# Performance work log

Hardware: AMD Instinct MI355X
Metric: run time of the kernel (lower is better)

Reference implementation:

```python
import jax, jax.numpy as jnp
import numpy as np

NEG_SLOPE = 0.01  # LeakyReLU default
STRIDE = 5        # group_length // 4
EPS = 1e-5        # RMSNorm eps


def leaky_relu(x):
    return jnp.where(x >= 0, x, NEG_SLOPE * x)


def rmsnorm(x, w):
    return x * jax.lax.rsqrt(jnp.mean(x * x, axis=-1, keepdims=True) + EPS) * w


def s6(x, fc1_w, fc1_b, fc2_w, fc2_b, fc3_w, fc3_b, A):
    # x: [B, L, D] with D = 2*d_model; A: [D, N]
    delta = jax.nn.softplus(x @ fc1_w.T + fc1_b)        # [B, L, D]
    Bm = x @ fc2_w.T + fc2_b                             # [B, L, N]
    Cm = x @ fc3_w.T + fc3_b                             # [B, L, N]
    dA = jnp.exp(jnp.einsum('bld,dn->bldn', delta, A))   # [B, L, D, N]
    dBx = jnp.einsum('bld,bln,bld->bldn', delta, Bm, x)  # delta * B * x

    def step(h, inp):
        dA_t, dBx_t = inp
        h = dA_t * h + dBx_t
        return h, h

    B_, L, D, N = dA.shape
    h0 = jnp.zeros((B_, D, N), dtype=x.dtype)
    _, hs = jax.lax.scan(step, h0, (jnp.swapaxes(dA, 0, 1), jnp.swapaxes(dBx, 0, 1)))
    hs = jnp.swapaxes(hs, 0, 1)                          # [B, L, D, N]
    return jnp.einsum('bln,bldn->bld', Cm, hs)           # [B, L, D]


def setup_inputs() -> dict:
    key = jax.random.key(0)
    ks = iter(jax.random.split(key, 32))

    def rn(shape, scale=0.02):
        return scale * jax.random.normal(next(ks), shape, dtype=jnp.float32)

    B, band, gl, d, N, L = 256, 189, 20, 128, 128, 34
    di = 2 * d
    return {
        'x': jax.random.normal(next(ks), (B, 1, band), dtype=jnp.float32),
        'conv_w': rn((d, 1, gl)), 'conv_b': rn((d,)),
        'norm_w': jnp.ones((d,), jnp.float32),
        'inp_w': rn((di, d)), 'inp_b': rn((di,)),
        'seqconv_w': rn((L, L, 3)), 'seqconv_b': rn((L,)),
        'convlin_w': rn((di, di)), 'convlin_b': rn((di,)),
        'fc1_w': rn((di, di)), 'fc1_b': rn((di,)),
        'fc2_w': rn((N, di)), 'fc2_b': rn((N,)),
        'fc3_w': rn((N, di)), 'fc3_b': rn((N,)),
        'A': jnp.ones((di, N), jnp.float32) / jnp.sqrt(jnp.float32(N)),
        'D_w': rn((di, d)), 'D_b': rn((di,)),
        'out_w': rn((d, di)), 'out_b': rn((d,)),
        'fnn1_w': rn((64, L * d)), 'fnn1_b': rn((64,)),
        'fnn2_w': rn((32, 64)), 'fnn2_b': rn((32,)),
    }


def reference(x, conv_w, conv_b, norm_w, inp_w, inp_b, seqconv_w, seqconv_b,
              convlin_w, convlin_b, fc1_w, fc1_b, fc2_w, fc2_b, fc3_w, fc3_b,
              A, D_w, D_b, out_w, out_b, fnn1_w, fnn1_b, fnn2_w, fnn2_b):
    # group division: Conv1d(1, d, k=20, stride=5) + LeakyReLU
    g = jax.lax.conv_general_dilated(x, conv_w, (STRIDE,), [(0, 0)],
                                     dimension_numbers=('NCH', 'OIH', 'NCH'))
    g = leaky_relu(g + conv_b[None, :, None])            # [B, d, L]
    h = jnp.swapaxes(g, 1, 2)                            # [B, L, d]
    # Mamba block
    xn = rmsnorm(h, norm_w)
    xp = xn @ inp_w.T + inp_b                            # [B, L, 2d]
    # Conv1d(seq_len, seq_len, k=3, pad=1): seq axis L is the channel dim
    xc = jax.lax.conv_general_dilated(xp, seqconv_w, (1,), [(1, 1)],
                                      dimension_numbers=('NCH', 'OIH', 'NCH'))
    xc = jax.nn.silu(xc + seqconv_b[None, :, None])
    xc = xc @ convlin_w.T + convlin_b                    # [B, L, 2d]
    xs = s6(xc, fc1_w, fc1_b, fc2_w, fc2_b, fc3_w, fc3_b, A)
    y = jax.nn.silu(xs) * jax.nn.silu(xn @ D_w.T + D_b)  # gated
    y = y @ out_w.T + out_b                              # [B, L, d]
    # FNN head
    f = y.reshape(y.shape[0], -1)                        # [B, L*d]
    f = leaky_relu(f @ fnn1_w.T + fnn1_b)
    return f @ fnn2_w.T + fnn2_b                         # [B, 32]
```

## Files before the change

kernel.cpp:

```cpp
#include <hip/hip_runtime.h>
#include <math.h>


#define NB    256
#define LL    34
#define DD    128
#define DI    256
#define NN    128
#define MM    (NB*LL)

using u16 = unsigned short;
typedef __attribute__((ext_vector_type(8))) short short8;
typedef __attribute__((ext_vector_type(4))) float f32x4;

__device__ __forceinline__ float silu_f(float x)  { return x / (1.f + __expf(-x)); }
__device__ __forceinline__ float softplus_f(float x) {
    return fmaxf(x, 0.f) + __logf(1.f + __expf(-fabsf(x)));
}
__device__ __forceinline__ float leaky_f(float x) { return (x >= 0.f) ? x : 0.01f * x; }

__device__ __forceinline__ u16 f2bf(float x) {
    unsigned u = __float_as_uint(x);
    return (u16)((u + 0x7FFF + ((u >> 16) & 1)) >> 16);
}
__device__ __forceinline__ float bf2f(u16 h) {
    return __uint_as_float(((unsigned)h) << 16);
}
__device__ __forceinline__ void f2pair(float v, u16* h, u16* l) {
    u16 hh = f2bf(v);
    *h = hh;
    *l = f2bf(v - bf2f(hh));
}

__global__ __launch_bounds__(256)
void prep_k(const float* __restrict__ inp_w, const float* __restrict__ D_w,
            const float* __restrict__ fc1_w, const float* __restrict__ fc2_w,
            const float* __restrict__ fc3_w, const float* __restrict__ convlin_w,
            const float* __restrict__ out_w,
            const float* __restrict__ inp_b, const float* __restrict__ D_b,
            const float* __restrict__ fc1_b, const float* __restrict__ fc2_b,
            const float* __restrict__ fc3_b,
            const float* __restrict__ W1, const float* __restrict__ A,
            u16* __restrict__ wc1h, u16* __restrict__ wc1l,
            u16* __restrict__ wc3h, u16* __restrict__ wc3l,
            u16* __restrict__ cvh,  u16* __restrict__ cvl,
            u16* __restrict__ owh,  u16* __restrict__ owl,
            float* __restrict__ bias1, float* __restrict__ bias3,
            float* __restrict__ W1T, int* __restrict__ flag)
{
    const int bx  = blockIdx.x;
    const int tid = threadIdx.x;
    __shared__ float tile[64][65];

    if (bx < 1152) {
        int i = bx * 256 + tid;
        if (i < 65536) {
            float v = (i < 32768) ? inp_w[i] : D_w[i - 32768];
            f2pair(v, &wc1h[i], &wc1l[i]);
        } else if (i < 196608) {
            int j = i - 65536;
            float v = (j < 65536) ? fc1_w[j] : (j < 98304 ? fc2_w[j - 65536] : fc3_w[j - 98304]);
            f2pair(v, &wc3h[j], &wc3l[j]);
        } else if (i < 262144) {
            int j = i - 196608;
            f2pair(convlin_w[j], &cvh[j], &cvl[j]);
        } else if (i < 294912) {
            int j = i - 262144;
            f2pair(out_w[j], &owh[j], &owl[j]);
        }
        if (i < 512)  bias1[i] = (i < 256) ? inp_b[i] : D_b[i - 256];
        else if (i < 1024) {
            int j = i - 512;
            bias3[j] = (j < 256) ? fc1_b[j] : (j < 384 ? fc2_b[j - 256] : fc3_b[j - 384]);
        }
    } else if (bx < 1220) {
        const int bt = bx - 1152;
        for (int p = 0; p < 16; p++) {
            int idx = tid + p * 256;
            int r = idx >> 6, c = idx & 63;
            tile[r][c] = W1[(size_t)r * 4352 + bt * 64 + c];
        }
        __syncthreads();
        for (int p = 0; p < 16; p++) {
            int idx = tid + p * 256;
            int cc = idx >> 6, rr = idx & 63;
            W1T[(size_t)(bt * 64 + cc) * 64 + rr] = tile[rr][cc];
        }
    } else {
        __shared__ int s;
        if (tid == 0) s = 1;
        __syncthreads();
        bool ok = true;
        for (int k = 0; k < 128; k++) {
            int idx = tid + k * 256;
            ok &= (A[idx] == A[idx & ~127]);
        }
        if (!ok) s = 0;
        __syncthreads();
        if (tid == 0) *flag = s;
    }
}

__global__ __launch_bounds__(1024, 1)
void mega2_k(const int* __restrict__ flag,
             const float* __restrict__ x,
             const float* __restrict__ cw, const float* __restrict__ cb,
             const float* __restrict__ nw,
             const u16* __restrict__ wc1h, const u16* __restrict__ wc1l,
             const float* __restrict__ bias1,
             const float* __restrict__ scw, const float* __restrict__ scb,
             const u16* __restrict__ cvh, const u16* __restrict__ cvl,
             const float* __restrict__ clb,
             const u16* __restrict__ wc3h, const u16* __restrict__ wc3l,
             const float* __restrict__ bias3,
             const float* __restrict__ A,
             const u16* __restrict__ owh, const u16* __restrict__ owl,
             const float* __restrict__ outb,
             float* __restrict__ buf1,
             float* __restrict__ buf3,
             u16* __restrict__ bcpair,
             u16* __restrict__ xc2h, u16* __restrict__ xc2l,
             float* __restrict__ fout)
{
    const int b    = blockIdx.x;
    const int tid  = threadIdx.x;
    const int wave = tid >> 6;
    const int lane = tid & 63;
    const int l15  = lane & 15;
    const int lq   = lane >> 4;

    __shared__ __align__(16) char smem[144944];
    float (*sx)[264] = (float (*)[264])(smem);
    float (*sw)[112] = (float (*)[112])(smem + 35904);
    u16 (*sXch)[264] = (u16 (*)[264])(smem);
    u16 (*sXcl)[264] = (u16 (*)[264])(smem + 25344);
    u16 (*sBh)[136]  = (u16 (*)[136])(smem);
    u16 (*sBl)[136]  = (u16 (*)[136])(smem + 13056);
    u16 (*sCh)[136]  = (u16 (*)[136])(smem + 26112);
    u16 (*sCl)[136]  = (u16 (*)[136])(smem + 39168);
    u16 (*sGh)[264]  = (u16 (*)[264])(smem);
    u16 (*sGl)[264]  = (u16 (*)[264])(smem + 25344);
    u16 (*sXnh)[136] = (u16 (*)[136])(smem + 52224);
    u16 (*sXnl)[136] = (u16 (*)[136])(smem + 65280);
    u16 (*sX2h)[264] = (u16 (*)[264])(smem + 52224);
    u16 (*sX2l)[264] = (u16 (*)[264])(smem + 77568);
    float (*sM)[49]  = (float (*)[49])(smem + 102912);
    float (*sDG)[260]= (float (*)[260])(smem + 109584);

    const bool uni = (*flag != 0);

    for (int idx = tid; idx < LL * LL * 3; idx += 1024) {
        int lo = idx / 102;
        int rem = idx - lo * 102;
        int li = rem / 3;
        int k  = rem - li * 3;
        sw[li][lo * 3 + k] = scw[idx];
    }
    if (tid < LL) { sx[tid][0] = 0.f; sx[tid][257] = 0.f; }

    {
        const int t = lane;
        #pragma unroll
        for (int pass = 0; pass < 3; pass++) {
            const int rr = pass * 16 + wave;
            if (rr < LL) {
                const float* xr = x + (size_t)b * 189 + rr * 5;
                float xv[20];
                #pragma unroll
                for (int k = 0; k < 20; k++) xv[k] = xr[k];
                float g0 = cb[t];
                float g1 = cb[t + 64];
                #pragma unroll
                for (int k = 0; k < 20; k++) {
                    g0 = fmaf(xv[k], cw[t * 20 + k], g0);
                    g1 = fmaf(xv[k], cw[(t + 64) * 20 + k], g1);
                }
                g0 = leaky_f(g0);
                g1 = leaky_f(g1);
                float s = fmaf(g1, g1, g0 * g0);
                #pragma unroll
                for (int m = 32; m >= 1; m >>= 1) s += __shfl_xor(s, m);
                float inv = 1.f / sqrtf(s * (1.f / 128.f) + 1e-5f);
                float v0 = g0 * inv * nw[t];
                float v1 = g1 * inv * nw[t + 64];
                f2pair(v0, &sXnh[rr][t], &sXnl[rr][t]);
                f2pair(v1, &sXnh[rr][t + 64], &sXnl[rr][t + 64]);
            }
        }
    }
    __syncthreads();

    {
        const int c0 = wave * 32;
        f32x4 a1[3][2];
        #pragma unroll
        for (int i = 0; i < 3; i++)
            #pragma unroll
            for (int j = 0; j < 2; j++) a1[i][j] = (f32x4){0.f, 0.f, 0.f, 0.f};

        #pragma unroll
        for (int ks = 0; ks < 4; ks++) {
            short8 fh[3], fl[3];
            #pragma unroll
            for (int i = 0; i < 3; i++) {
                fh[i] = *(const short8*)&sXnh[i * 16 + l15][ks * 32 + lq * 8];
                fl[i] = *(const short8*)&sXnl[i * 16 + l15][ks * 32 + lq * 8];
            }
            #pragma unroll
            for (int j = 0; j < 2; j++) {
                const size_t wo = (size_t)(c0 + j * 16 + l15) * 128 + ks * 32 + lq * 8;
                short8 bh = *(const short8*)&wc1h[wo];
                short8 bl = *(const short8*)&wc1l[wo];
                #pragma unroll
                for (int i = 0; i < 3; i++) {
                    a1[i][j] = __builtin_amdgcn_mfma_f32_16x16x32_bf16(fh[i], bh, a1[i][j], 0, 0, 0);
                    a1[i][j] = __builtin_amdgcn_mfma_f32_16x16x32_bf16(fh[i], bl, a1[i][j], 0, 0, 0);
                    a1[i][j] = __builtin_amdgcn_mfma_f32_16x16x32_bf16(fl[i], bh, a1[i][j], 0, 0, 0);
                }
            }
        }
        #pragma unroll
        for (int i = 0; i < 3; i++) {
            int row = i * 16 + lq * 4;
            #pragma unroll
            for (int j = 0; j < 2; j++) {
                int col = c0 + j * 16 + l15;
                float bb = bias1[col];
                #pragma unroll
                for (int r = 0; r < 4; r++) {
                    float v = a1[i][j][r] + bb;
                    int rr = row + r;
                    if (rr < LL) {
                        if (col < 256) {
                            sx[rr][col + 1] = v;
                        } else {
                            sDG[rr][col - 256] = v;
                            if (!uni)
                                buf1[((size_t)b * LL + rr) * 512 + col] = v;
                        }
                    }
                }
            }
        }
    }
    __syncthreads();

    {
        const int tx  = tid & 63;
        const int ty  = tid >> 6;
        const int j0c = tx * 4;
        const int cbase = (ty < 2) ? ty * 3 : 6 + (ty - 2) * 2;
        const int ccnt  = (ty < 2) ? 3 : 2;

        float cacc[3][4];
        #pragma unroll
        for (int i = 0; i < 3; i++)
            #pragma unroll
            for (int jj = 0; jj < 4; jj++) cacc[i][jj] = 0.f;

        for (int li = 0; li < LL; li++) {
            float4 xa = *(const float4*)&sx[li][j0c];
            float2 xb = *(const float2*)&sx[li][j0c + 4];
            float xv[6] = {xa.x, xa.y, xa.z, xa.w, xb.x, xb.y};
            const float* swr = &sw[li][0];
            #pragma unroll
            for (int i = 0; i < 3; i++) {
                if (i < ccnt) {
                    int lo3 = (cbase + i) * 3;
                    float w0 = swr[lo3 + 0];
                    float w1 = swr[lo3 + 1];
                    float w2 = swr[lo3 + 2];
                    #pragma unroll
                    for (int jj = 0; jj < 4; jj++) {
                        cacc[i][jj] = fmaf(w0, xv[jj],     cacc[i][jj]);
                        cacc[i][jj] = fmaf(w1, xv[jj + 1], cacc[i][jj]);
                        cacc[i][jj] = fmaf(w2, xv[jj + 2], cacc[i][jj]);
                    }
                }
            }
        }
        __syncthreads();

        #pragma unroll
        for (int i = 0; i < 3; i++) {
            if (i < ccnt) {
                int lo = cbase + i;
                float bb = scb[lo];
                ushort4 oh, ol;
                float v0 = silu_f(cacc[i][0] + bb);
                float v1 = silu_f(cacc[i][1] + bb);
                float v2 = silu_f(cacc[i][2] + bb);
                float v3 = silu_f(cacc[i][3] + bb);
                f2pair(v0, &oh.x, &ol.x);
                f2pair(v1, &oh.y, &ol.y);
                f2pair(v2, &oh.z, &ol.z);
                f2pair(v3, &oh.w, &ol.w);
                *(ushort4*)&sXch[lo][j0c] = oh;
                *(ushort4*)&sXcl[lo][j0c] = ol;
            }
        }
    }
    __syncthreads();

    {
        const int c0 = wave * 16;
        f32x4 a2[3];
        #pragma unroll
        for (int i = 0; i < 3; i++) a2[i] = (f32x4){0.f, 0.f, 0.f, 0.f};

        #pragma unroll
        for (int ks = 0; ks < 8; ks++) {
            short8 fh[3], fl[3];
            #pragma unroll
            for (int i = 0; i < 3; i++) {
                fh[i] = *(const short8*)&sXch[i * 16 + l15][ks * 32 + lq * 8];
                fl[i] = *(const short8*)&sXcl[i * 16 + l15][ks * 32 + lq * 8];
            }
            const size_t wo = (size_t)(c0 + l15) * 256 + ks * 32 + lq * 8;
            short8 bh = *(const short8*)&cvh[wo];
            short8 bl = *(const short8*)&cvl[wo];
            #pragma unroll
            for (int i = 0; i < 3; i++) {
                a2[i] = __builtin_amdgcn_mfma_f32_16x16x32_bf16(fh[i], bh, a2[i], 0, 0, 0);
                a2[i] = __builtin_amdgcn_mfma_f32_16x16x32_bf16(fh[i], bl, a2[i], 0, 0, 0);
                a2[i] = __builtin_amdgcn_mfma_f32_16x16x32_bf16(fl[i], bh, a2[i], 0, 0, 0);
            }
        }
        #pragma unroll
        for (int i = 0; i < 3; i++) {
            int row = i * 16 + lq * 4;
            int col = c0 + l15;
            float bb = clb[col];
            #pragma unroll
            for (int r = 0; r < 4; r++) {
                float v = a2[i][r] + bb;
                u16 hh, ll;
                f2pair(v, &hh, &ll);
                sX2h[row + r][col] = hh;
                sX2l[row + r][col] = ll;
                if (!uni && (row + r) < LL) {
                    xc2h[(size_t)(b * LL + row + r) * 256 + col] = hh;
                    xc2l[(size_t)(b * LL + row + r) * 256 + col] = ll;
                }
            }
        }
    }
    __syncthreads();

    {
        const int c0 = wave * 32;
        f32x4 a3[3][2];
        #pragma unroll
        for (int i = 0; i < 3; i++)
            #pragma unroll
            for (int j = 0; j < 2; j++) a3[i][j] = (f32x4){0.f, 0.f, 0.f, 0.f};

        #pragma unroll
        for (int ks = 0; ks < 8; ks++) {
            short8 fh[3], fl[3];
            #pragma unroll
            for (int i = 0; i < 3; i++) {
                fh[i] = *(const short8*)&sX2h[i * 16 + l15][ks * 32 + lq * 8];
                fl[i] = *(const short8*)&sX2l[i * 16 + l15][ks * 32 + lq * 8];
            }
            #pragma unroll
            for (int j = 0; j < 2; j++) {
                const size_t wo = (size_t)(c0 + j * 16 + l15) * 256 + ks * 32 + lq * 8;
                short8 bh = *(const short8*)&wc3h[wo];
                short8 bl = *(const short8*)&wc3l[wo];
                #pragma unroll
                for (int i = 0; i < 3; i++) {
                    a3[i][j] = __builtin_amdgcn_mfma_f32_16x16x32_bf16(fh[i], bh, a3[i][j], 0, 0, 0);
                    a3[i][j] = __builtin_amdgcn_mfma_f32_16x16x32_bf16(fh[i], bl, a3[i][j], 0, 0, 0);
                    a3[i][j] = __builtin_amdgcn_mfma_f32_16x16x32_bf16(fl[i], bh, a3[i][j], 0, 0, 0);
                }
            }
        }
        #pragma unroll
        for (int i = 0; i < 3; i++) {
            int row = i * 16 + lq * 4;
            #pragma unroll
            for (int j = 0; j < 2; j++) {
                int col = c0 + j * 16 + l15;
                float bb = bias3[col];
                #pragma unroll
                for (int r = 0; r < 4; r++) {
                    float v = a3[i][j][r] + bb;
                    int rr = row + r;
                    if (col < 256) {
                        v = softplus_f(v);
                        if (rr < LL) buf3[((size_t)b * LL + rr) * 512 + col] = v;
                    } else {
                        u16 hh, ll;
                        f2pair(v, &hh, &ll);
                        int cc = col & 127;
                        if (col < 384) { sBh[rr][cc] = hh; sBl[rr][cc] = ll; }
                        else           { sCh[rr][cc] = hh; sCl[rr][cc] = ll; }
                        if (!uni && rr < LL) {
                            buf3[((size_t)b * LL + rr) * 512 + col] = v;
                            u16* rb = bcpair + ((size_t)b * LL + rr) * 1024
                                      + ((col < 384) ? 0 : 256) + cc;
                            rb[0]   = hh;
                            rb[128] = ll;
                        }
                    }
                }
            }
        }
    }
    __syncthreads();
    if (!uni) return;

    float u[LL], eS[LL];
    if (tid < 256) {
        const int d = tid;
        const float a_d = A[(size_t)d * NN];
        const float* pDel = buf3 + (size_t)b * LL * 512 + d;
        float S = 0.f;
        #pragma unroll
        for (int l = 0; l < LL; l++) {
            float dl = pDel[l * 512];
            S = fmaf(dl, a_d, S);
            eS[l] = __expf(S);
            float xv = bf2f(sX2h[l][d]) + bf2f(sX2l[l][d]);
            u[l] = __expf(-S) * dl * xv;
        }
    } else if (wave >= 4 && wave < 13) {
        int tt = wave - 4;
        int ti = tt / 3, tj = tt - ti * 3;
        f32x4 acc = (f32x4){0.f, 0.f, 0.f, 0.f};
        #pragma unroll
        for (int ks = 0; ks < 4; ks++) {
            short8 ch = *(const short8*)&sCh[ti * 16 + l15][ks * 32 + lq * 8];
            short8 cl = *(const short8*)&sCl[ti * 16 + l15][ks * 32 + lq * 8];
            short8 bh = *(const short8*)&sBh[tj * 16 + l15][ks * 32 + lq * 8];
            short8 bl = *(const short8*)&sBl[tj * 16 + l15][ks * 32 + lq * 8];
            acc = __builtin_amdgcn_mfma_f32_16x16x32_bf16(ch, bh, acc, 0, 0, 0);
            acc = __builtin_amdgcn_mfma_f32_16x16x32_bf16(ch, bl, acc, 0, 0, 0);
            acc = __builtin_amdgcn_mfma_f32_16x16x32_bf16(cl, bh, acc, 0, 0, 0);
        }
        #pragma unroll
        for (int r = 0; r < 4; r++) {
            int row = ti * 16 + lq * 4 + r;
            if (row < LL) sM[row][tj * 16 + l15] = acc[r];
        }
    }
    __syncthreads();

    if (tid < 256) {
        const int d = tid;
        #pragma unroll
        for (int l = 0; l < LL; l++) {
            float acc = 0.f;
            for (int t = 0; t <= l; t++) acc = fmaf(sM[l][t], u[t], acc);
            float xs = eS[l] * acc;
            float g = silu_f(xs) * silu_f(sDG[l][d]);
            u16 hh, ll2;
            f2pair(g, &hh, &ll2);
            sGh[l][d] = hh;
            sGl[l][d] = ll2;
        }
    } else {
        u16* zh = &sGh[34][0];
        u16* zl = &sGl[34][0];
        for (int idx = tid - 256; idx < 14 * 264; idx += 768) {
            zh[idx] = 0;
            zl[idx] = 0;
        }
    }
    __syncthreads();

    {
        const int j0 = wave & 7;
        const int i0 = (wave >> 3) ? 2 : 0;
        const int ni = (wave >> 3) ? 1 : 2;
        f32x4 a4[2];
        #pragma unroll
        for (int i = 0; i < 2; i++) a4[i] = (f32x4){0.f, 0.f, 0.f, 0.f};
        #pragma unroll
        for (int ks = 0; ks < 8; ks++) {
            const size_t wo = (size_t)(j0 * 16 + l15) * 256 + ks * 32 + lq * 8;
            short8 bh = *(const short8*)&owh[wo];
            short8 bl = *(const short8*)&owl[wo];
            #pragma unroll
            for (int i = 0; i < 2; i++) {
                if (i < ni) {
                    short8 ah = *(const short8*)&sGh[(i0 + i) * 16 + l15][ks * 32 + lq * 8];
                    short8 al = *(const short8*)&sGl[(i0 + i) * 16 + l15][ks * 32 + lq * 8];
                    a4[i] = __builtin_amdgcn_mfma_f32_16x16x32_bf16(ah, bh, a4[i], 0, 0, 0);
                    a4[i] = __builtin_amdgcn_mfma_f32_16x16x32_bf16(ah, bl, a4[i], 0, 0, 0);
                    a4[i] = __builtin_amdgcn_mfma_f32_16x16x32_bf16(al, bh, a4[i], 0, 0, 0);
                }
            }
        }
        #pragma unroll
        for (int i = 0; i < 2; i++) {
            if (i < ni) {
                int row = (i0 + i) * 16 + lq * 4;
                int col = j0 * 16 + l15;
                float bb = outb[col];
                #pragma unroll
                for (int r = 0; r < 4; r++)
                    if (row + r < LL)
                        fout[(size_t)(b * LL + row + r) * 128 + col] = a4[i][r] + bb;
            }
        }
    }
}

__global__ __launch_bounds__(256)
void scan_fb_k(const int* __restrict__ flag,
               const float* __restrict__ dBC,
               const u16*  __restrict__ Xh, const u16* __restrict__ Xl,
               const float* __restrict__ A,
               const float* __restrict__ DG,
               u16* __restrict__ Gh, u16* __restrict__ Gl)
{
    if (*flag != 0) return;
    const int b  = blockIdx.y;
    const int d0 = blockIdx.x * 64;
    const int tid = threadIdx.x;
    const int sub = tid & 15;
    const int pg  = tid >> 4;
    const int dbase = d0 + pg * 4;
    const int nA = sub * 4;

    float a[4][8], h[4][8];
    #pragma unroll
    for (int dd = 0; dd < 4; dd++) {
        const float* Ar = A + (size_t)(dbase + dd) * NN;
        float4 q0 = *(const float4*)(Ar + nA);
        float4 q1 = *(const float4*)(Ar + 64 + nA);
        a[dd][0]=q0.x; a[dd][1]=q0.y; a[dd][2]=q0.z; a[dd][3]=q0.w;
        a[dd][4]=q1.x; a[dd][5]=q1.y; a[dd][6]=q1.z; a[dd][7]=q1.w;
        #pragma unroll
        for (int j = 0; j < 8; j++) h[dd][j] = 0.f;
    }

    const float* pD  = dBC + (size_t)b * LL * 512 + dbase;
    const float* pBC = dBC + (size_t)b * LL * 512 + 256 + nA;
    const u16*  pXh = Xh  + (size_t)b * LL * 256 + dbase;
    const u16*  pXl = Xl  + (size_t)b * LL * 256 + dbase;
    const float* pG  = DG  + (size_t)b * LL * 512 + 256 + dbase;
    u16* pGh = Gh + (size_t)b * LL * 256 + dbase;
    u16* pGl = Gl + (size_t)b * LL * 256 + dbase;

    for (int l = 0; l < LL; l++) {
        float4  cD  = *(const float4*)(pD);
        ushort4 cXh = *(const ushort4*)(pXh);
        ushort4 cXl = *(const ushort4*)(pXl);
        float4 cB0 = *(const float4*)(pBC);
        float4 cB1 = *(const float4*)(pBC + 64);
        float4 cC0 = *(const float4*)(pBC + 128);
        float4 cC1 = *(const float4*)(pBC + 192);
        pD += 512; pBC += 512; pXh += 256; pXl += 256;

        float xv[4] = { bf2f(cXh.x) + bf2f(cXl.x), bf2f(cXh.y) + bf2f(cXl.y),
                        bf2f(cXh.z) + bf2f(cXl.z), bf2f(cXh.w) + bf2f(cXl.w) };
        float dl[4] = {cD.x, cD.y, cD.z, cD.w};
        float dx[4] = {cD.x * xv[0], cD.y * xv[1], cD.z * xv[2], cD.w * xv[3]};
        float bv[8] = {cB0.x,cB0.y,cB0.z,cB0.w,cB1.x,cB1.y,cB1.z,cB1.w};
        float cv[8] = {cC0.x,cC0.y,cC0.z,cC0.w,cC1.x,cC1.y,cC1.z,cC1.w};

        float accd[4] = {0.f, 0.f, 0.f, 0.f};
        #pragma unroll
        for (int dd = 0; dd < 4; dd++)
            #pragma unroll
            for (int j = 0; j < 8; j++) {
                float dA = __expf(dl[dd] * a[dd][j]);
                h[dd][j] = fmaf(dA, h[dd][j], dx[dd] * bv[j]);
                accd[dd] = fmaf(cv[j], h[dd][j], accd[dd]);
            }
        #pragma unroll
        for (int dd = 0; dd < 4; dd++) {
            float v = accd[dd];
            v += __shfl_xor(v, 1);
            v += __shfl_xor(v, 2);
            v += __shfl_xor(v, 4);
            v += __shfl_xor(v, 8);
            accd[dd] = v;
        }
        if (sub == 0) {
            float4 dg = *(const float4*)(pG);
            ushort4 oh, ol;
            float g0 = silu_f(accd[0]) * silu_f(dg.x);
            float g1 = silu_f(accd[1]) * silu_f(dg.y);
            float g2 = silu_f(accd[2]) * silu_f(dg.z);
            float g3 = silu_f(accd[3]) * silu_f(dg.w);
            f2pair(g0, &oh.x, &ol.x);
            f2pair(g1, &oh.y, &ol.y);
            f2pair(g2, &oh.z, &ol.z);
            f2pair(g3, &oh.w, &ol.w);
            *(ushort4*)pGh = oh;
            *(ushort4*)pGl = ol;
        }
        pG += 512; pGh += 256; pGl += 256;
    }
}

__global__ __launch_bounds__(512)
void tail_cold_k(const int* __restrict__ flag,
                 const u16* __restrict__ gFh, const u16* __restrict__ gFl,
                 const u16* __restrict__ owh, const u16* __restrict__ owl,
                 const float* __restrict__ outb,
                 float* __restrict__ fout)
{
    if (*flag != 0) return;
    const int b    = blockIdx.x;
    const int tid  = threadIdx.x;
    const int wave = tid >> 6;
    const int lane = tid & 63;
    const int l15  = lane & 15;
    const int lq   = lane >> 4;

    __shared__ u16 sGh[48][264];
    __shared__ u16 sGl[48][264];

    for (int idx = tid; idx < LL * 32; idx += 512) {
        int l = idx >> 5, c = (idx & 31) << 3;
        *(short8*)&sGh[l][c] = *(const short8*)&gFh[((size_t)b * LL + l) * 256 + c];
        *(short8*)&sGl[l][c] = *(const short8*)&gFl[((size_t)b * LL + l) * 256 + c];
    }
    {
        u16* zh = &sGh[34][0];
        u16* zl = &sGl[34][0];
        for (int idx = tid; idx < 14 * 264; idx += 512) {
            zh[idx] = 0;
            zl[idx] = 0;
        }
    }
    __syncthreads();

    const int j0 = wave;
    f32x4 a4[3];
    #pragma unroll
    for (int i = 0; i < 3; i++) a4[i] = (f32x4){0.f, 0.f, 0.f, 0.f};
    #pragma unroll
    for (int ks = 0; ks < 8; ks++) {
        const size_t wo = (size_t)(j0 * 16 + l15) * 256 + ks * 32 + lq * 8;
        short8 bh = *(const short8*)&owh[wo];
        short8 bl = *(const short8*)&owl[wo];
        #pragma unroll
        for (int i = 0; i < 3; i++) {
            short8 ah = *(const short8*)&sGh[i * 16 + l15][ks * 32 + lq * 8];
            short8 al = *(const short8*)&sGl[i * 16 + l15][ks * 32 + lq * 8];
            a4[i] = __builtin_amdgcn_mfma_f32_16x16x32_bf16(ah, bh, a4[i], 0, 0, 0);
            a4[i] = __builtin_amdgcn_mfma_f32_16x16x32_bf16(ah, bl, a4[i], 0, 0, 0);
            a4[i] = __builtin_amdgcn_mfma_f32_16x16x32_bf16(al, bh, a4[i], 0, 0, 0);
        }
    }
    #pragma unroll
    for (int i = 0; i < 3; i++) {
        int row = i * 16 + lq * 4;
        int col = j0 * 16 + l15;
        float bb = outb[col];
        #pragma unroll
        for (int r = 0; r < 4; r++)
            if (row + r < LL)
                fout[(size_t)(b * LL + row + r) * 128 + col] = a4[i][r] + bb;
    }
}

__global__ __launch_bounds__(256)
void fnn1_k(const float* __restrict__ F, const float* __restrict__ W1T,
            float* __restrict__ partials)
{
    const int btile = blockIdx.x;
    const int kc    = blockIdx.y;
    const int tid   = threadIdx.x;
    __shared__ float sf[16][260];
    for (int i = tid; i < 16 * 256; i += 256) {
        int r = i >> 8, c = i & 255;
        sf[r][c] = F[(size_t)(btile * 16 + r) * 4352 + kc * 256 + c];
    }
    __syncthreads();

    const int o  = tid & 63;
    const int bq = tid >> 6;
    const float* w = W1T + (size_t)(kc * 256) * 64 + o;
    float acc[4] = {0.f, 0.f, 0.f, 0.f};
    for (int k = 0; k < 256; k += 4) {
        float w0 = w[(size_t)(k + 0) * 64];
        float w1 = w[(size_t)(k + 1) * 64];
        float w2 = w[(size_t)(k + 2) * 64];
        float w3 = w[(size_t)(k + 3) * 64];
        #pragma unroll
        for (int bj = 0; bj < 4; bj++) {
            float4 f4 = *(const float4*)&sf[bq * 4 + bj][k];
            acc[bj] = fmaf(w0, f4.x, acc[bj]);
            acc[bj] = fmaf(w1, f4.y, acc[bj]);
            acc[bj] = fmaf(w2, f4.z, acc[bj]);
            acc[bj] = fmaf(w3, f4.w, acc[bj]);
        }
    }
    #pragma unroll
    for (int bj = 0; bj < 4; bj++)
        partials[(size_t)kc * 16384 + (btile * 16 + bq * 4 + bj) * 64 + o] = acc[bj];
}

__global__ __launch_bounds__(64)
void fnn2_k(const float* __restrict__ partials,
            const float* __restrict__ B1,
            const float* __restrict__ W2, const float* __restrict__ B2,
            float* __restrict__ out)
{
    int b = blockIdx.x;
    int t = threadIdx.x;
    __shared__ float s1[64];
    float acc = B1[t];
    #pragma unroll
    for (int kc = 0; kc < 17; kc++)
        acc += partials[(size_t)kc * 16384 + b * 64 + t];
    s1[t] = leaky_f(acc);
    __syncthreads();

    if (t < 32) {
        float acc2 = B2[t];
        const float* w2 = W2 + t * 64;
        #pragma unroll
        for (int j = 0; j < 64; j++) acc2 = fmaf(s1[j], w2[j], acc2);
        out[(size_t)b * 32 + t] = acc2;
    }
}

extern "C" void kernel_launch(void* const* d_in, const int* in_sizes, int n_in,
                              void* d_out, int out_size, void* d_ws, size_t ws_size,
                              hipStream_t stream)
{
    const float* x        = (const float*)d_in[0];
    const float* conv_w   = (const float*)d_in[1];
    const float* conv_b   = (const float*)d_in[2];
    const float* norm_w   = (const float*)d_in[3];
    const float* inp_w    = (const float*)d_in[4];
    const float* inp_b    = (const float*)d_in[5];
    const float* seqconv_w= (const float*)d_in[6];
    const float* seqconv_b= (const float*)d_in[7];
    const float* convlin_w= (const float*)d_in[8];
    const float* convlin_b= (const float*)d_in[9];
    const float* fc1_w    = (const float*)d_in[10];
    const float* fc1_b    = (const float*)d_in[11];
    const float* fc2_w    = (const float*)d_in[12];
    const float* fc2_b    = (const float*)d_in[13];
    const float* fc3_w    = (const float*)d_in[14];
    const float* fc3_b    = (const float*)d_in[15];
    const float* A        = (const float*)d_in[16];
    const float* D_w      = (const float*)d_in[17];
    const float* D_b      = (const float*)d_in[18];
    const float* out_w    = (const float*)d_in[19];
    const float* out_b    = (const float*)d_in[20];
    const float* fnn1_w   = (const float*)d_in[21];
    const float* fnn1_b   = (const float*)d_in[22];
    const float* fnn2_w   = (const float*)d_in[23];
    const float* fnn2_b   = (const float*)d_in[24];

    char* W = (char*)d_ws;
    float* buf1  = (float*)(W + 0);
    float* buf3  = (float*)(W + 17825792);
    float* fout  = (float*)(W + 35651584);
    u16*   xc2h  = (u16*)  (W + 37879808);
    u16*   xc2l  = (u16*)  (W + 42336256);
    u16*   gateh = (u16*)  (W + 44564480);
    u16*   gatel = (u16*)  (W + 49020928);
    float* w1t   = (float*)(W + 53477376);
    u16*   wc1h  = (u16*)  (W + 54591488);
    u16*   wc1l  = (u16*)  (W + 54722560);
    u16*   wc3h  = (u16*)  (W + 54853632);
    u16*   wc3l  = (u16*)  (W + 55115776);
    u16*   cvh   = (u16*)  (W + 55377920);
    u16*   cvl   = (u16*)  (W + 55508992);
    u16*   owh   = (u16*)  (W + 55640064);
    u16*   owl   = (u16*)  (W + 55705600);
    float* bias1 = (float*)(W + 55771136);
    float* bias3 = (float*)(W + 55773184);
    int*   uflag = (int*)  (W + 55775232);
    u16* bcpair = (u16*)buf1;
    float* partials = buf3;

    prep_k<<<1221, 256, 0, stream>>>(inp_w, D_w, fc1_w, fc2_w, fc3_w,
                                     convlin_w, out_w,
                                     inp_b, D_b, fc1_b, fc2_b, fc3_b,
                                     fnn1_w, A,
                                     wc1h, wc1l, wc3h, wc3l, cvh, cvl,
                                     owh, owl, bias1, bias3, w1t, uflag);

    mega2_k<<<NB, 1024, 0, stream>>>(uflag, x, conv_w, conv_b, norm_w,
                                     wc1h, wc1l, bias1,
                                     seqconv_w, seqconv_b,
                                     cvh, cvl, convlin_b, wc3h, wc3l, bias3,
                                     A, owh, owl, out_b,
                                     buf1, buf3, bcpair, xc2h, xc2l, fout);

    scan_fb_k<<<dim3(4, NB), 256, 0, stream>>>(uflag, buf3, xc2h, xc2l, A,
                                               buf1, gateh, gatel);
    tail_cold_k<<<NB, 512, 0, stream>>>(uflag, gateh, gatel, owh, owl, out_b,
                                        fout);

    fnn1_k<<<dim3(16, 17), 256, 0, stream>>>(fout, w1t, partials);
    fnn2_k<<<NB, 64, 0, stream>>>(partials, fnn1_b, fnn2_w, fnn2_b,
                                  (float*)d_out);
}
```

Before: 198.4 us.

## Move FNN1 head GEMM onto bf16 split-precision MFMA

The FNN1 projection (256x4352 by 4352x64) now runs on MFMA using a three-term bf16 hi/lo split instead of scalar FP32 FMAs. The output projection writes its result as bf16 hi/lo pairs, and prep_k converts fnn1_w to hi/lo pairs in place of its transpose. fnn1_k loads operands straight from global memory with no LDS staging and runs on a smaller grid (4x17 blocks). The trade is a bit of extra precision loss and fewer blocks in exchange for cheaper arithmetic, on top of a larger weight-preparation pass.

After: 202.3 us. No clear change (+2.0%).

```diff
diff --git a/kernel.cpp b/kernel.cpp
--- a/kernel.cpp
+++ b/kernel.cpp
@@ -45,14 +45,14 @@
             u16* __restrict__ wc3h, u16* __restrict__ wc3l,
             u16* __restrict__ cvh,  u16* __restrict__ cvl,
             u16* __restrict__ owh,  u16* __restrict__ owl,
+            u16* __restrict__ w1h,  u16* __restrict__ w1l,
             float* __restrict__ bias1, float* __restrict__ bias3,
-            float* __restrict__ W1T, int* __restrict__ flag)
+            int* __restrict__ flag)
 {
     const int bx  = blockIdx.x;
     const int tid = threadIdx.x;
-    __shared__ float tile[64][65];
-
-    if (bx < 1152) {
+
+    if (bx < 2240) {
         int i = bx * 256 + tid;
         if (i < 65536) {
             float v = (i < 32768) ? inp_w[i] : D_w[i - 32768];
@@ -67,24 +67,14 @@
         } else if (i < 294912) {
             int j = i - 262144;
             f2pair(out_w[j], &owh[j], &owl[j]);
+        } else if (i < 573440) {
+            int j = i - 294912;
+            f2pair(W1[j], &w1h[j], &w1l[j]);
         }
         if (i < 512)  bias1[i] = (i < 256) ? inp_b[i] : D_b[i - 256];
         else if (i < 1024) {
             int j = i - 512;
             bias3[j] = (j < 256) ? fc1_b[j] : (j < 384 ? fc2_b[j - 256] : fc3_b[j - 384]);
-        }
-    } else if (bx < 1220) {
-        const int bt = bx - 1152;
-        for (int p = 0; p < 16; p++) {
-            int idx = tid + p * 256;
-            int r = idx >> 6, c = idx & 63;
-            tile[r][c] = W1[(size_t)r * 4352 + bt * 64 + c];
-        }
-        __syncthreads();
-        for (int p = 0; p < 16; p++) {
-            int idx = tid + p * 256;
-            int cc = idx >> 6, rr = idx & 63;
-            W1T[(size_t)(bt * 64 + cc) * 64 + rr] = tile[rr][cc];
         }
     } else {
         __shared__ int s;
@@ -120,7 +110,7 @@
              float* __restrict__ buf3,
              u16* __restrict__ bcpair,
              u16* __restrict__ xc2h, u16* __restrict__ xc2l,
-             float* __restrict__ fout)
+             u16* __restrict__ Fh, u16* __restrict__ Fl)
 {
     const int b    = blockIdx.x;
     const int tid  = threadIdx.x;
@@ -501,8 +491,14 @@
                 float bb = outb[col];
                 #pragma unroll
                 for (int r = 0; r < 4; r++)
-                    if (row + r < LL)
-                        fout[(size_t)(b * LL + row + r) * 128 + col] = a4[i][r] + bb;
+                    if (row + r < LL) {
+                        float v = a4[i][r] + bb;
+                        u16 hh, ll;
+                        f2pair(v, &hh, &ll);
+                        size_t fo = (size_t)b * 4352 + (row + r) * 128 + col;
+                        Fh[fo] = hh;
+                        Fl[fo] = ll;
+                    }
             }
         }
     }
@@ -603,7 +599,7 @@
                  const u16* __restrict__ gFh, const u16* __restrict__ gFl,
                  const u16* __restrict__ owh, const u16* __restrict__ owl,
                  const float* __restrict__ outb,
-                 float* __restrict__ fout)
+                 u16* __restrict__ Fh, u16* __restrict__ Fl)
 {
     if (*flag != 0) return;
     const int b    = blockIdx.x;
@@ -656,46 +652,56 @@
         float bb = outb[col];
         #pragma unroll
         for (int r = 0; r < 4; r++)
-            if (row + r < LL)
-                fout[(size_t)(b * LL + row + r) * 128 + col] = a4[i][r] + bb;
+            if (row + r < LL) {
+                float v = a4[i][r] + bb;
+                u16 hh, ll;
+                f2pair(v, &hh, &ll);
+                size_t fo = (size_t)b * 4352 + (row + r) * 128 + col;
+                Fh[fo] = hh;
+                Fl[fo] = ll;
+            }
     }
 }
 
 __global__ __launch_bounds__(256)
-void fnn1_k(const float* __restrict__ F, const float* __restrict__ W1T,
+void fnn1_k(const u16* __restrict__ Fh, const u16* __restrict__ Fl,
+            const u16* __restrict__ w1h, const u16* __restrict__ w1l,
             float* __restrict__ partials)
 {
-    const int btile = blockIdx.x;
-    const int kc    = blockIdx.y;
-    const int tid   = threadIdx.x;
-    __shared__ float sf[16][260];
-    for (int i = tid; i < 16 * 256; i += 256) {
-        int r = i >> 8, c = i & 255;
-        sf[r][c] = F[(size_t)(btile * 16 + r) * 4352 + kc * 256 + c];
-    }
-    __syncthreads();
-
-    const int o  = tid & 63;
-    const int bq = tid >> 6;
-    const float* w = W1T + (size_t)(kc * 256) * 64 + o;
-    float acc[4] = {0.f, 0.f, 0.f, 0.f};
-    for (int k = 0; k < 256; k += 4) {
-        float w0 = w[(size_t)(k + 0) * 64];
-        float w1 = w[(size_t)(k + 1) * 64];
-        float w2 = w[(size_t)(k + 2) * 64];
-        float w3 = w[(size_t)(k + 3) * 64];
-        #pragma unroll
-        for (int bj = 0; bj < 4; bj++) {
-            float4 f4 = *(const float4*)&sf[bq * 4 + bj][k];
-            acc[bj] = fmaf(w0, f4.x, acc[bj]);
-            acc[bj] = fmaf(w1, f4.y, acc[bj]);
-            acc[bj] = fmaf(w2, f4.z, acc[bj]);
-            acc[bj] = fmaf(w3, f4.w, acc[bj]);
-        }
-    }
+    const int mt   = blockIdx.x;
+    const int kc   = blockIdx.y;
+    const int wave = threadIdx.x >> 6;
+    const int lane = threadIdx.x & 63;
+    const int l15  = lane & 15;
+    const int lq   = lane >> 4;
+
+    f32x4 acc[4];
     #pragma unroll
-    for (int bj = 0; bj < 4; bj++)
-        partials[(size_t)kc * 16384 + (btile * 16 + bq * 4 + bj) * 64 + o] = acc[bj];
+    for (int i = 0; i < 4; i++) acc[i] = (f32x4){0.f, 0.f, 0.f, 0.f};
+
+    #pragma unroll
+    for (int ks = 0; ks < 8; ks++) {
+        const size_t wo = (size_t)(wave * 16 + l15) * 4352 + kc * 256 + ks * 32 + lq * 8;
+        short8 bh = *(const short8*)&w1h[wo];
+        short8 bl = *(const short8*)&w1l[wo];
+        #pragma unroll
+        for (int i = 0; i < 4; i++) {
+            const size_t ao = (size_t)(mt * 64 + i * 16 + l15) * 4352 + kc * 256 + ks * 32 + lq * 8;
+            short8 ah = *(const short8*)&Fh[ao];
+            short8 al = *(const short8*)&Fl[ao];
+            acc[i] = __builtin_amdgcn_mfma_f32_16x16x32_bf16(ah, bh, acc[i], 0, 0, 0);
+            acc[i] = __builtin_amdgcn_mfma_f32_16x16x32_bf16(ah, bl, acc[i], 0, 0, 0);
+            acc[i] = __builtin_amdgcn_mfma_f32_16x16x32_bf16(al, bh, acc[i], 0, 0, 0);
+        }
+    }
+    #pragma unroll
+    for (int i = 0; i < 4; i++) {
+        int row = mt * 64 + i * 16 + lq * 4;
+        int col = wave * 16 + l15;
+        #pragma unroll
+        for (int r = 0; r < 4; r++)
+            partials[(size_t)kc * 16384 + (row + r) * 64 + col] = acc[i][r];
+    }
 }
 
 __global__ __launch_bounds__(64)
@@ -756,46 +762,48 @@
     char* W = (char*)d_ws;
     float* buf1  = (float*)(W + 0);
     float* buf3  = (float*)(W + 17825792);
-    float* fout  = (float*)(W + 35651584);
-    u16*   xc2h  = (u16*)  (W + 37879808);
-    u16*   xc2l  = (u16*)  (W + 42336256);
-    u16*   gateh = (u16*)  (W + 44564480);
-    u16*   gatel = (u16*)  (W + 49020928);
-    float* w1t   = (float*)(W + 53477376);
-    u16*   wc1h  = (u16*)  (W + 54591488);
-    u16*   wc1l  = (u16*)  (W + 54722560);
-    u16*   wc3h  = (u16*)  (W + 54853632);
-    u16*   wc3l  = (u16*)  (W + 55115776);
-    u16*   cvh   = (u16*)  (W + 55377920);
-    u16*   cvl   = (u16*)  (W + 55508992);
-    u16*   owh   = (u16*)  (W + 55640064);
-    u16*   owl   = (u16*)  (W + 55705600);
-    float* bias1 = (float*)(W + 55771136);
-    float* bias3 = (float*)(W + 55773184);
-    int*   uflag = (int*)  (W + 55775232);
+    u16*   Fh    = (u16*)  (W + 35651584);
+    u16*   Fl    = (u16*)  (W + 37879808);
+    u16*   xc2h  = (u16*)  (W + 40108032);
+    u16*   xc2l  = (u16*)  (W + 44564480);
+    u16*   gateh = (u16*)  (W + 49020928);
+    u16*   gatel = (u16*)  (W + 53477376);
+    u16*   w1h   = (u16*)  (W + 57933824);
+    u16*   w1l   = (u16*)  (W + 58490880);
+    u16*   wc1h  = (u16*)  (W + 59047936);
+    u16*   wc1l  = (u16*)  (W + 59179008);
+    u16*   wc3h  = (u16*)  (W + 59310080);
+    u16*   wc3l  = (u16*)  (W + 59572224);
+    u16*   cvh   = (u16*)  (W + 59834368);
+    u16*   cvl   = (u16*)  (W + 59965440);
+    u16*   owh   = (u16*)  (W + 60096512);
+    u16*   owl   = (u16*)  (W + 60162048);
+    float* bias1 = (float*)(W + 60227584);
+    float* bias3 = (float*)(W + 60229632);
+    int*   uflag = (int*)  (W + 60231680);
     u16* bcpair = (u16*)buf1;
     float* partials = buf3;
 
-    prep_k<<<1221, 256, 0, stream>>>(inp_w, D_w, fc1_w, fc2_w, fc3_w,
+    prep_k<<<2241, 256, 0, stream>>>(inp_w, D_w, fc1_w, fc2_w, fc3_w,
                                      convlin_w, out_w,
                                      inp_b, D_b, fc1_b, fc2_b, fc3_b,
                                      fnn1_w, A,
                                      wc1h, wc1l, wc3h, wc3l, cvh, cvl,
-                                     owh, owl, bias1, bias3, w1t, uflag);
+                                     owh, owl, w1h, w1l, bias1, bias3, uflag);
 
     mega2_k<<<NB, 1024, 0, stream>>>(uflag, x, conv_w, conv_b, norm_w,
                                      wc1h, wc1l, bias1,
                                      seqconv_w, seqconv_b,
                                      cvh, cvl, convlin_b, wc3h, wc3l, bias3,
                                      A, owh, owl, out_b,
-                                     buf1, buf3, bcpair, xc2h, xc2l, fout);
+                                     buf1, buf3, bcpair, xc2h, xc2l, Fh, Fl);
 
     scan_fb_k<<<dim3(4, NB), 256, 0, stream>>>(uflag, buf3, xc2h, xc2l, A,
                                                buf1, gateh, gatel);
     tail_cold_k<<<NB, 512, 0, stream>>>(uflag, gateh, gatel, owh, owl, out_b,
-                                        fout);
-
-    fnn1_k<<<dim3(16, 17), 256, 0, stream>>>(fout, w1t, partials);
+                                        Fh, Fl);
+
+    fnn1_k<<<dim3(4, 17), 256, 0, stream>>>(Fh, Fl, w1h, w1l, partials);
     fnn2_k<<<NB, 64, 0, stream>>>(partials, fnn1_b, fnn2_w, fnn2_b,
                                   (float*)d_out);
 }
```
